# Kernel tuning notes

Hardware: AMD Instinct MI355X
Metric: run time of the kernel (lower is better)

Reference implementation:

```python
import jax, jax.numpy as jnp
import numpy as np
from jax import lax

B, CIN, COUT, H, W = 4, 256, 256, 64, 64
K, DG, STRIDE, PAD, DIL = 3, 1, 1, 1, 1
K2 = K * K
CG = CIN // DG
HO = (H + 2 * PAD - DIL * (K - 1) - 1) // STRIDE + 1
WO = (W + 2 * PAD - DIL * (K - 1) - 1) // STRIDE + 1


def setup_inputs() -> dict:
    key = jax.random.key(0)
    k1, k2, k3 = jax.random.split(key, 3)
    inputs = jax.random.normal(k1, (B, CIN, H, W), jnp.float32)
    # original init_offset() zeros these; small random weights instead so offsets ~0.5px
    w_off = jax.random.normal(k2, (3 * DG * K2, CIN, K, K), jnp.float32) * 0.01
    b_off = jnp.zeros((3 * DG * K2,), jnp.float32)
    w_dcn = jax.random.normal(k3, (COUT, CIN, K, K), jnp.float32) * (1.0 / np.sqrt(CIN * K2))
    b_dcn = jnp.zeros((COUT,), jnp.float32)
    return {"inputs": inputs, "w_off": w_off, "b_off": b_off, "w_dcn": w_dcn, "b_dcn": b_dcn}


def _conv2d(x, w, b):
    y = lax.conv_general_dilated(x, w, (STRIDE, STRIDE), [(PAD, PAD), (PAD, PAD)],
                                 rhs_dilation=(DIL, DIL),
                                 dimension_numbers=("NCHW", "OIHW", "NCHW"))
    return y + b[None, :, None, None]


def _dcn_forward(inputs, w_off, b_off, w_dcn, b_dcn):
    # offset/mask branch (standard conv), then chunk into o1, o2, mask
    om = _conv2d(inputs, w_off, b_off)                      # [B, 3*DG*K2, HO, WO]
    o1, o2, m = jnp.split(om, 3, axis=1)
    offset = jnp.concatenate([o1, o2], axis=1)              # [B, 2*DG*K2, HO, WO]
    mask = jax.nn.sigmoid(m)                                # [B, DG*K2, HO, WO]

    # DCNv2 offset layout: per deformable group, K2 taps of (dy, dx)
    off = offset.reshape(B, DG, K2, 2, HO, WO)
    dy, dx = off[:, :, :, 0], off[:, :, :, 1]               # [B, DG, K2, HO, WO]

    taps = jnp.arange(K2)
    ki = (taps // K).astype(jnp.float32)
    kj = (taps % K).astype(jnp.float32)
    hb = (jnp.arange(HO, dtype=jnp.float32) * STRIDE - PAD)
    wb = (jnp.arange(WO, dtype=jnp.float32) * STRIDE - PAD)
    py = dy + hb[None, None, None, :, None] + (ki * DIL)[None, None, :, None, None]
    px = dx + wb[None, None, None, None, :] + (kj * DIL)[None, None, :, None, None]

    y0f, x0f = jnp.floor(py), jnp.floor(px)
    ly, lx = py - y0f, px - x0f
    y0, x0 = y0f.astype(jnp.int32), x0f.astype(jnp.int32)
    y1, x1 = y0 + 1, x0 + 1

    flat = inputs.reshape(B, DG, CG, H * W)

    def corner(yi, xi, wgt):
        valid = (yi >= 0) & (yi < H) & (xi >= 0) & (xi < W)
        yc = jnp.clip(yi, 0, H - 1)
        xc = jnp.clip(xi, 0, W - 1)
        idx = (yc * W + xc).reshape(B, DG, 1, K2 * HO * WO)
        idx = jnp.broadcast_to(idx, (B, DG, CG, K2 * HO * WO))
        v = jnp.take_along_axis(flat, idx, axis=3).reshape(B, DG, CG, K2, HO, WO)
        w = jnp.where(valid, wgt, 0.0)[:, :, None]          # zero outside (zero-pad bilinear)
        return v * w

    val = (corner(y0, x0, (1 - ly) * (1 - lx)) + corner(y0, x1, (1 - ly) * lx)
           + corner(y1, x0, ly * (1 - lx)) + corner(y1, x1, ly * lx))

    cols = val * mask.reshape(B, DG, 1, K2, HO, WO)         # modulated columns
    cols = cols.reshape(B, CIN * K2, HO * WO)
    out = jnp.einsum("ok,bkn->bon", w_dcn.reshape(COUT, CIN * K2), cols)
    out = out + b_dcn[None, :, None]
    return out.reshape(B, COUT, HO, WO)


def reference(inputs, w_off, b_off, w_dcn, b_dcn):
    return _dcn_forward(inputs, w_off, b_off, w_dcn, b_dcn)
```

## Files before the change

kernel.cpp:

```cpp
#include <hip/hip_runtime.h>
#include <hip/hip_bf16.h>

typedef __bf16 bf16x8 __attribute__((ext_vector_type(8)));
typedef __bf16 bf16x4 __attribute__((ext_vector_type(4)));
typedef float f32x4 __attribute__((ext_vector_type(4)));
typedef unsigned int u32x4 __attribute__((ext_vector_type(4)));

#define CIN 256
#define COUT 256
#define KDIM 2304

__device__ __forceinline__ void gload_lds16(const void* g, void* l) {
  __builtin_amdgcn_global_load_lds(
      (__attribute__((address_space(1))) unsigned int*)g,
      (__attribute__((address_space(3))) unsigned int*)l, 16, 0, 0);
}

__global__ __launch_bounds__(256) void k_prep_all(const float* __restrict__ wdcn,
                                                  const float* __restrict__ woff,
                                                  __bf16* __restrict__ Ag,
                                                  __bf16* __restrict__ Ah,
                                                  __bf16* __restrict__ Al) {
  int bid = blockIdx.x, tid = threadIdx.x;
  if (bid < 2304) {
    int t = bid * 256 + tid;
    int cout = t / KDIM;
    int r = t - cout * KDIM;
    int tap = r >> 8, cin = r & 255;
    Ag[t] = (__bf16)wdcn[(cout * 256 + cin) * 9 + tap];
  } else {
    int t = (bid - 2304) * 256 + tid;
    int j = t & 7;
    int l = (t >> 3) & 63;
    int mh = (t >> 9) & 1;
    int s = t >> 10;
    int tap = s >> 3, cc = s & 7;
    int ki = tap / 3, kj = tap - ki * 3;
    int oc = mh * 16 + (l & 15);
    int cin = cc * 32 + ((l >> 4) << 3) + j;
    float v = (oc < 27) ? woff[((oc * 256 + cin) * 3 + ki) * 3 + kj] : 0.f;
    __bf16 hi = (__bf16)v;
    __bf16 lo = (__bf16)(v - (float)hi);
    Ah[t] = hi;
    Al[t] = lo;
  }
}

__global__ __launch_bounds__(256) void k_tr(const float* __restrict__ in,
                                            __bf16* __restrict__ inT) {
  int h = blockIdx.x, b = blockIdx.y;
  int c = threadIdx.x;
  const float* src = in + ((((b << 8) + c) << 6) + h) * 64;
  __bf16* dst = inT + (((b << 12) + (h << 6)) << 8) + c;
#pragma unroll
  for (int w4 = 0; w4 < 16; ++w4) {
    f32x4 v = *(const f32x4*)(src + (w4 << 2));
#pragma unroll
    for (int k = 0; k < 4; ++k) dst[(((w4 << 2) + k)) << 8] = (__bf16)v[k];
  }
}

__global__ __launch_bounds__(256) void k_conv(const float* __restrict__ in,
                                              const __bf16* __restrict__ Ah,
                                              const __bf16* __restrict__ Al,
                                              float* __restrict__ omp) {
  __shared__ __bf16 xh[3 * 4 * 66 * 8];
  __shared__ __bf16 xl[3 * 4 * 66 * 8];
  int tid = threadIdx.x;
  int l = tid & 63, wn = tid >> 6;
  int ho = blockIdx.x, b = blockIdx.y, ct = blockIdx.z;

  f32x4 acc[2];
  acc[0] = (f32x4){0.f, 0.f, 0.f, 0.f};
  acc[1] = (f32x4){0.f, 0.f, 0.f, 0.f};

  for (int chunk = 0; chunk < 4; ++chunk) {
    int cin0 = ct * 128 + chunk * 32;
    for (int i = tid; i < 792; i += 256) {
      int c = i % 66;
      int t2 = i / 66;
      int u = t2 & 3, r = t2 >> 2;
      int h = ho - 1 + r, w = c - 1;
      bool ok = ((unsigned)h < 64u) & ((unsigned)w < 64u);
      const float* src = in + ((((b * CIN + cin0 + u * 8) << 6) + h) << 6) + w;
      bf16x8 hv, lv;
#pragma unroll
      for (int k = 0; k < 8; ++k) {
        float v = ok ? src[k << 12] : 0.f;
        __bf16 hi = (__bf16)v;
        hv[k] = hi;
        lv[k] = (__bf16)(v - (float)hi);
      }
      int el = ((r * 4 + u) * 66 + c) << 3;
      *(bf16x8*)&xh[el] = hv;
      *(bf16x8*)&xl[el] = lv;
    }
    __syncthreads();
    int scc = ct * 4 + chunk;
#pragma unroll
    for (int tap = 0; tap < 9; ++tap) {
      int s = tap * 8 + scc;
      int ki = tap / 3, kj = tap - ki * 3;
      bf16x8 ah0 = *(const bf16x8*)(Ah + (((s * 2 + 0) * 64 + l) << 3));
      bf16x8 ah1 = *(const bf16x8*)(Ah + (((s * 2 + 1) * 64 + l) << 3));
      bf16x8 al0 = *(const bf16x8*)(Al + (((s * 2 + 0) * 64 + l) << 3));
      bf16x8 al1 = *(const bf16x8*)(Al + (((s * 2 + 1) * 64 + l) << 3));
      int u = l >> 4;
      int sc = (wn << 4) + (l & 15) + kj;
      int el = ((ki * 4 + u) * 66 + sc) << 3;
      bf16x8 bh = *(const bf16x8*)&xh[el];
      bf16x8 bl = *(const bf16x8*)&xl[el];
      acc[0] = __builtin_amdgcn_mfma_f32_16x16x32_bf16(ah0, bh, acc[0], 0, 0, 0);
      acc[1] = __builtin_amdgcn_mfma_f32_16x16x32_bf16(ah1, bh, acc[1], 0, 0, 0);
      acc[0] = __builtin_amdgcn_mfma_f32_16x16x32_bf16(al0, bh, acc[0], 0, 0, 0);
      acc[1] = __builtin_amdgcn_mfma_f32_16x16x32_bf16(al1, bh, acc[1], 0, 0, 0);
      acc[0] = __builtin_amdgcn_mfma_f32_16x16x32_bf16(ah0, bl, acc[0], 0, 0, 0);
      acc[1] = __builtin_amdgcn_mfma_f32_16x16x32_bf16(ah1, bl, acc[1], 0, 0, 0);
    }
    __syncthreads();
  }
  int n = (ho << 6) + (wn << 4) + (l & 15);
#pragma unroll
  for (int mh = 0; mh < 2; ++mh)
#pragma unroll
    for (int r = 0; r < 4; ++r) {
      int oc = mh * 16 + ((l >> 4) << 2) + r;
      if (oc < 27)
        omp[(((ct * 4 + b) * 27 + oc) << 12) + n] = acc[mh][r];
    }
}

__global__ __launch_bounds__(512, 4) void k_gemm(const __bf16* __restrict__ inT,
                                                 const float* __restrict__ omp,
                                                 const float* __restrict__ boff,
                                                 const __bf16* __restrict__ Ag,
                                                 const float* __restrict__ bdcn,
                                                 float* __restrict__ out) {
  __shared__ u32x4 sA[2048];
  __shared__ u32x4 sB[256];
  int tid = threadIdx.x;
  int l = tid & 63;
  int w = tid >> 6;
  int wm = w & 3, wh = w >> 2;
  int id = blockIdx.x;
  int x = id & 7, t = id >> 3;
  int b = x >> 1;
  int ntile = ((x & 1) << 6) + t;
  int sn = tid >> 4;
  int sc = tid & 15;
  int n_g = (ntile << 5) + sn;
  const __bf16* tb = inT + ((b << 12) << 8);

  f32x4 acc[4];
#pragma unroll
  for (int i = 0; i < 4; ++i) acc[i] = (f32x4){0.f, 0.f, 0.f, 0.f};

  float w00 = 0.f, w01 = 0.f, w10 = 0.f, w11 = 0.f;
  int o00 = 0, o01 = 0, o10 = 0, o11 = 0;

  for (int step = 0; step < 36; ++step) {
    int tap = step >> 2;
    int cin0 = (step & 3) << 6;
    if ((step & 3) == 0) {
      int ki = tap / 3, kj = tap - ki * 3;
      float dy = omp[((b * 27 + 2 * tap) << 12) + n_g] +
                 omp[(((4 + b) * 27 + 2 * tap) << 12) + n_g] + boff[2 * tap];
      float dx = omp[((b * 27 + 2 * tap + 1) << 12) + n_g] +
                 omp[(((4 + b) * 27 + 2 * tap + 1) << 12) + n_g] + boff[2 * tap + 1];
      float mv = omp[((b * 27 + 18 + tap) << 12) + n_g] +
                 omp[(((4 + b) * 27 + 18 + tap) << 12) + n_g] + boff[18 + tap];
      float msk = 1.f / (1.f + __expf(-mv));
      float py = dy + (float)((n_g >> 6) - 1 + ki);
      float px = dx + (float)((n_g & 63) - 1 + kj);
      float y0f = floorf(py), x0f = floorf(px);
      float ly = py - y0f, lx = px - x0f;
      int y0 = (int)y0f, x0 = (int)x0f;
      int y1 = y0 + 1, x1 = x0 + 1;
      bool vy0 = (y0 >= 0) & (y0 < 64), vy1 = (y1 >= 0) & (y1 < 64);
      bool vx0 = (x0 >= 0) & (x0 < 64), vx1 = (x1 >= 0) & (x1 < 64);
      float hy = 1.f - ly, hx = 1.f - lx;
      w00 = (vy0 & vx0) ? hy * hx * msk : 0.f;
      w01 = (vy0 & vx1) ? hy * lx * msk : 0.f;
      w10 = (vy1 & vx0) ? ly * hx * msk : 0.f;
      w11 = (vy1 & vx1) ? ly * lx * msk : 0.f;
      int y0c = min(max(y0, 0), 63), y1c = min(max(y1, 0), 63);
      int x0c = min(max(x0, 0), 63), x1c = min(max(x1, 0), 63);
      o00 = (y0c << 6) + x0c;
      o01 = (y0c << 6) + x1c;
      o10 = (y1c << 6) + x0c;
      o11 = (y1c << 6) + x1c;
    }
    int cbase = cin0 + (sc << 2);
    bf16x4 cA = *(const bf16x4*)(tb + (o00 << 8) + cbase);
    bf16x4 cB = *(const bf16x4*)(tb + (o01 << 8) + cbase);
    bf16x4 cC = *(const bf16x4*)(tb + (o10 << 8) + cbase);
    bf16x4 cD = *(const bf16x4*)(tb + (o11 << 8) + cbase);
    bf16x4 vv;
#pragma unroll
    for (int j = 0; j < 4; ++j) {
      float v = w00 * (float)cA[j] + w01 * (float)cB[j] + w10 * (float)cC[j] +
                w11 * (float)cD[j];
      vv[j] = (__bf16)v;
    }
    __syncthreads();
    int kk0 = (tap << 8) + cin0;
#pragma unroll
    for (int i = 0; i < 4; ++i) {
      int slot = i * 512 + tid;
      int m = slot >> 3, j = slot & 7;
      int csrc = j ^ (m & 7);
      const __bf16* src = Ag + m * KDIM + kk0 + (csrc << 3);
      gload_lds16((const void*)src, (void*)&sA[i * 512 + (tid & ~63)]);
    }
    {
      unsigned long long* sB64 = (unsigned long long*)sB;
      int slot = (sn << 3) + ((sc >> 1) ^ (sn & 7));
      sB64[slot * 2 + (sc & 1)] = __builtin_bit_cast(unsigned long long, vv);
    }
    __syncthreads();
#pragma unroll
    for (int kt = 0; kt < 2; ++kt) {
      bf16x8 af[4], bfr;
      int cc = (kt << 2) + (l >> 4);
#pragma unroll
      for (int mf = 0; mf < 4; ++mf) {
        int m = (wm << 6) + (mf << 4) + (l & 15);
        af[mf] = __builtin_bit_cast(bf16x8, sA[(m << 3) + (cc ^ (m & 7))]);
      }
      {
        int n = (wh << 4) + (l & 15);
        bfr = __builtin_bit_cast(bf16x8, sB[(n << 3) + (cc ^ (n & 7))]);
      }
#pragma unroll
      for (int mf = 0; mf < 4; ++mf)
        acc[mf] = __builtin_amdgcn_mfma_f32_16x16x32_bf16(af[mf], bfr, acc[mf],
                                                          0, 0, 0);
    }
  }
#pragma unroll
  for (int mf = 0; mf < 4; ++mf)
#pragma unroll
    for (int r = 0; r < 4; ++r) {
      int m = (wm << 6) + (mf << 4) + ((l >> 4) << 2) + r;
      int n = (ntile << 5) + (wh << 4) + (l & 15);
      out[((b * COUT + m) << 12) + n] = acc[mf][r] + bdcn[m];
    }
}

extern "C" void kernel_launch(void* const* d_in, const int* in_sizes, int n_in,
                              void* d_out, int out_size, void* d_ws, size_t ws_size,
                              hipStream_t stream) {
  const float* in = (const float*)d_in[0];
  const float* woff = (const float*)d_in[1];
  const float* boff = (const float*)d_in[2];
  const float* wdcn = (const float*)d_in[3];
  const float* bdcn = (const float*)d_in[4];
  float* out = (float*)d_out;
  char* ws = (char*)d_ws;
  __bf16* Ag = (__bf16*)ws;
  __bf16* Ah = (__bf16*)(ws + 1179648);
  __bf16* Al = (__bf16*)(ws + 1327104);
  float* omp = (float*)(ws + 1474560);
  __bf16* inT = (__bf16*)(ws + 5013504);
  k_prep_all<<<2592, 256, 0, stream>>>(wdcn, woff, Ag, Ah, Al);
  k_tr<<<dim3(64, 4), 256, 0, stream>>>(in, inT);
  k_conv<<<dim3(64, 4, 2), 256, 0, stream>>>(in, Ah, Al, omp);
  k_gemm<<<512, 512, 0, stream>>>(inT, omp, boff, Ag, bdcn, out);
}
```

Before: 93.61 us.

## Double-buffer weight tile in LDS and prefetch next-step gathers during MFMA

Doubles the shared-memory A buffer so that the next K-step's weight tile is loaded into the alternate buffer while the current step's MFMAs run. The bilinear corner gathers and offset/mask computation for the next step are also issued before the MFMA loop, so their latency overlaps with math. The second __syncthreads is replaced by an explicit lgkmcnt wait plus a raw s_barrier with scheduling barriers. In exchange, LDS per block roughly doubles, which may cut the number of resident 512-thread blocks per CU. Vector memory waits are still forced at the top-of-loop barrier, which limits how much overlap is achieved.

```diff
diff --git a/kernel.cpp b/kernel.cpp
--- a/kernel.cpp
+++ b/kernel.cpp
@@ -136,7 +136,7 @@
                                                  const __bf16* __restrict__ Ag,
                                                  const float* __restrict__ bdcn,
                                                  float* __restrict__ out) {
-  __shared__ u32x4 sA[2048];
+  __shared__ u32x4 sA[2 * 2048];
   __shared__ u32x4 sB[256];
   int tid = threadIdx.x;
   int l = tid & 63;
@@ -157,67 +157,84 @@
 
   float w00 = 0.f, w01 = 0.f, w10 = 0.f, w11 = 0.f;
   int o00 = 0, o01 = 0, o10 = 0, o11 = 0;
-
-  for (int step = 0; step < 36; ++step) {
-    int tap = step >> 2;
-    int cin0 = (step & 3) << 6;
-    if ((step & 3) == 0) {
-      int ki = tap / 3, kj = tap - ki * 3;
-      float dy = omp[((b * 27 + 2 * tap) << 12) + n_g] +
-                 omp[(((4 + b) * 27 + 2 * tap) << 12) + n_g] + boff[2 * tap];
-      float dx = omp[((b * 27 + 2 * tap + 1) << 12) + n_g] +
-                 omp[(((4 + b) * 27 + 2 * tap + 1) << 12) + n_g] + boff[2 * tap + 1];
-      float mv = omp[((b * 27 + 18 + tap) << 12) + n_g] +
-                 omp[(((4 + b) * 27 + 18 + tap) << 12) + n_g] + boff[18 + tap];
-      float msk = 1.f / (1.f + __expf(-mv));
-      float py = dy + (float)((n_g >> 6) - 1 + ki);
-      float px = dx + (float)((n_g & 63) - 1 + kj);
-      float y0f = floorf(py), x0f = floorf(px);
-      float ly = py - y0f, lx = px - x0f;
-      int y0 = (int)y0f, x0 = (int)x0f;
-      int y1 = y0 + 1, x1 = x0 + 1;
-      bool vy0 = (y0 >= 0) & (y0 < 64), vy1 = (y1 >= 0) & (y1 < 64);
-      bool vx0 = (x0 >= 0) & (x0 < 64), vx1 = (x1 >= 0) & (x1 < 64);
-      float hy = 1.f - ly, hx = 1.f - lx;
-      w00 = (vy0 & vx0) ? hy * hx * msk : 0.f;
-      w01 = (vy0 & vx1) ? hy * lx * msk : 0.f;
-      w10 = (vy1 & vx0) ? ly * hx * msk : 0.f;
-      w11 = (vy1 & vx1) ? ly * lx * msk : 0.f;
-      int y0c = min(max(y0, 0), 63), y1c = min(max(y1, 0), 63);
-      int x0c = min(max(x0, 0), 63), x1c = min(max(x1, 0), 63);
-      o00 = (y0c << 6) + x0c;
-      o01 = (y0c << 6) + x1c;
-      o10 = (y1c << 6) + x0c;
-      o11 = (y1c << 6) + x1c;
-    }
-    int cbase = cin0 + (sc << 2);
-    bf16x4 cA = *(const bf16x4*)(tb + (o00 << 8) + cbase);
-    bf16x4 cB = *(const bf16x4*)(tb + (o01 << 8) + cbase);
-    bf16x4 cC = *(const bf16x4*)(tb + (o10 << 8) + cbase);
-    bf16x4 cD = *(const bf16x4*)(tb + (o11 << 8) + cbase);
-    bf16x4 vv;
-#pragma unroll
-    for (int j = 0; j < 4; ++j) {
-      float v = w00 * (float)cA[j] + w01 * (float)cB[j] + w10 * (float)cC[j] +
-                w11 * (float)cD[j];
-      vv[j] = (__bf16)v;
-    }
-    __syncthreads();
-    int kk0 = (tap << 8) + cin0;
+  bf16x4 cA, cB, cC, cD;
+
+  auto do_corners = [&](int tap) {
+    int ki = tap / 3, kj = tap - ki * 3;
+    float dy = omp[((b * 27 + 2 * tap) << 12) + n_g] +
+               omp[(((4 + b) * 27 + 2 * tap) << 12) + n_g] + boff[2 * tap];
+    float dx = omp[((b * 27 + 2 * tap + 1) << 12) + n_g] +
+               omp[(((4 + b) * 27 + 2 * tap + 1) << 12) + n_g] + boff[2 * tap + 1];
+    float mv = omp[((b * 27 + 18 + tap) << 12) + n_g] +
+               omp[(((4 + b) * 27 + 18 + tap) << 12) + n_g] + boff[18 + tap];
+    float msk = 1.f / (1.f + __expf(-mv));
+    float py = dy + (float)((n_g >> 6) - 1 + ki);
+    float px = dx + (float)((n_g & 63) - 1 + kj);
+    float y0f = floorf(py), x0f = floorf(px);
+    float ly = py - y0f, lx = px - x0f;
+    int y0 = (int)y0f, x0 = (int)x0f;
+    int y1 = y0 + 1, x1 = x0 + 1;
+    bool vy0 = (y0 >= 0) & (y0 < 64), vy1 = (y1 >= 0) & (y1 < 64);
+    bool vx0 = (x0 >= 0) & (x0 < 64), vx1 = (x1 >= 0) & (x1 < 64);
+    float hy = 1.f - ly, hx = 1.f - lx;
+    w00 = (vy0 & vx0) ? hy * hx * msk : 0.f;
+    w01 = (vy0 & vx1) ? hy * lx * msk : 0.f;
+    w10 = (vy1 & vx0) ? ly * hx * msk : 0.f;
+    w11 = (vy1 & vx1) ? ly * lx * msk : 0.f;
+    int y0c = min(max(y0, 0), 63), y1c = min(max(y1, 0), 63);
+    int x0c = min(max(x0, 0), 63), x1c = min(max(x1, 0), 63);
+    o00 = (y0c << 6) + x0c;
+    o01 = (y0c << 6) + x1c;
+    o10 = (y1c << 6) + x0c;
+    o11 = (y1c << 6) + x1c;
+  };
+  auto do_gather = [&](int s1) {
+    int cbase = ((s1 & 3) << 6) + (sc << 2);
+    cA = *(const bf16x4*)(tb + (o00 << 8) + cbase);
+    cB = *(const bf16x4*)(tb + (o01 << 8) + cbase);
+    cC = *(const bf16x4*)(tb + (o10 << 8) + cbase);
+    cD = *(const bf16x4*)(tb + (o11 << 8) + cbase);
+  };
+  auto do_stageA = [&](int s1, int p) {
+    int kk0 = ((s1 >> 2) << 8) + ((s1 & 3) << 6);
 #pragma unroll
     for (int i = 0; i < 4; ++i) {
       int slot = i * 512 + tid;
       int m = slot >> 3, j = slot & 7;
       int csrc = j ^ (m & 7);
       const __bf16* src = Ag + m * KDIM + kk0 + (csrc << 3);
-      gload_lds16((const void*)src, (void*)&sA[i * 512 + (tid & ~63)]);
-    }
+      gload_lds16((const void*)src, (void*)&sA[p * 2048 + i * 512 + (tid & ~63)]);
+    }
+  };
+
+  do_corners(0);
+  do_stageA(0, 0);
+  do_gather(0);
+
+  for (int s = 0; s < 36; ++s) {
+    bf16x4 vv;
+#pragma unroll
+    for (int j = 0; j < 4; ++j) {
+      float v = w00 * (float)cA[j] + w01 * (float)cB[j] + w10 * (float)cC[j] +
+                w11 * (float)cD[j];
+      vv[j] = (__bf16)v;
+    }
+    __syncthreads();
+    int s1 = (s < 35) ? s + 1 : 35;
+    do_stageA(s1, (s + 1) & 1);
     {
       unsigned long long* sB64 = (unsigned long long*)sB;
       int slot = (sn << 3) + ((sc >> 1) ^ (sn & 7));
       sB64[slot * 2 + (sc & 1)] = __builtin_bit_cast(unsigned long long, vv);
     }
-    __syncthreads();
+    asm volatile("s_waitcnt lgkmcnt(0)" ::: "memory");
+    __builtin_amdgcn_sched_barrier(0);
+    __builtin_amdgcn_s_barrier();
+    __builtin_amdgcn_sched_barrier(0);
+    if (((s + 1) & 3) == 0 && s < 35) do_corners((s + 1) >> 2);
+    do_gather(s1);
+    __builtin_amdgcn_sched_barrier(0);
+    int pb = (s & 1) * 2048;
 #pragma unroll
     for (int kt = 0; kt < 2; ++kt) {
       bf16x8 af[4], bfr;
@@ -225,7 +242,7 @@
 #pragma unroll
       for (int mf = 0; mf < 4; ++mf) {
         int m = (wm << 6) + (mf << 4) + (l & 15);
-        af[mf] = __builtin_bit_cast(bf16x8, sA[(m << 3) + (cc ^ (m & 7))]);
+        af[mf] = __builtin_bit_cast(bf16x8, sA[pb + (m << 3) + (cc ^ (m & 7))]);
       }
       {
         int n = (wh << 4) + (l & 15);
```

Result: slower. 98.29 us (+5.0%).

## Feed offset conv from bf16 transposed input and drop low-part input split

Applied to the files above, without the earlier changes.

The offset/mask convolution now reads the already-transposed bf16 channel-last input (inT) with one 16-byte load per site instead of eight strided fp32 loads. It also no longer splits the input into hi/lo bf16 parts, which removes one LDS buffer and two of the six MFMAs per tap. The aim is less global and LDS traffic and fewer matrix ops in the conv kernel. In exchange the offsets lose precision because the input is now only bf16, which can move sampling positions. k_conv now also has to run after k_tr.

```diff
diff --git a/kernel.cpp b/kernel.cpp
--- a/kernel.cpp
+++ b/kernel.cpp
@@ -60,12 +60,11 @@
   }
 }
 
-__global__ __launch_bounds__(256) void k_conv(const float* __restrict__ in,
+__global__ __launch_bounds__(256) void k_conv(const __bf16* __restrict__ inT,
                                               const __bf16* __restrict__ Ah,
                                               const __bf16* __restrict__ Al,
                                               float* __restrict__ omp) {
   __shared__ __bf16 xh[3 * 4 * 66 * 8];
-  __shared__ __bf16 xl[3 * 4 * 66 * 8];
   int tid = threadIdx.x;
   int l = tid & 63, wn = tid >> 6;
   int ho = blockIdx.x, b = blockIdx.y, ct = blockIdx.z;
@@ -82,18 +81,11 @@
       int u = t2 & 3, r = t2 >> 2;
       int h = ho - 1 + r, w = c - 1;
       bool ok = ((unsigned)h < 64u) & ((unsigned)w < 64u);
-      const float* src = in + ((((b * CIN + cin0 + u * 8) << 6) + h) << 6) + w;
-      bf16x8 hv, lv;
-#pragma unroll
-      for (int k = 0; k < 8; ++k) {
-        float v = ok ? src[k << 12] : 0.f;
-        __bf16 hi = (__bf16)v;
-        hv[k] = hi;
-        lv[k] = (__bf16)(v - (float)hi);
-      }
-      int el = ((r * 4 + u) * 66 + c) << 3;
-      *(bf16x8*)&xh[el] = hv;
-      *(bf16x8*)&xl[el] = lv;
+      bf16x8 hv = (bf16x8){};
+      if (ok)
+        hv = *(const bf16x8*)(inT + ((((b << 12) + (h << 6) + w)) << 8) + cin0 +
+                              (u << 3));
+      *(bf16x8*)&xh[((r * 4 + u) * 66 + c) << 3] = hv;
     }
     __syncthreads();
     int scc = ct * 4 + chunk;
@@ -107,15 +99,11 @@
       bf16x8 al1 = *(const bf16x8*)(Al + (((s * 2 + 1) * 64 + l) << 3));
       int u = l >> 4;
       int sc = (wn << 4) + (l & 15) + kj;
-      int el = ((ki * 4 + u) * 66 + sc) << 3;
-      bf16x8 bh = *(const bf16x8*)&xh[el];
-      bf16x8 bl = *(const bf16x8*)&xl[el];
+      bf16x8 bh = *(const bf16x8*)&xh[((ki * 4 + u) * 66 + sc) << 3];
       acc[0] = __builtin_amdgcn_mfma_f32_16x16x32_bf16(ah0, bh, acc[0], 0, 0, 0);
       acc[1] = __builtin_amdgcn_mfma_f32_16x16x32_bf16(ah1, bh, acc[1], 0, 0, 0);
       acc[0] = __builtin_amdgcn_mfma_f32_16x16x32_bf16(al0, bh, acc[0], 0, 0, 0);
       acc[1] = __builtin_amdgcn_mfma_f32_16x16x32_bf16(al1, bh, acc[1], 0, 0, 0);
-      acc[0] = __builtin_amdgcn_mfma_f32_16x16x32_bf16(ah0, bl, acc[0], 0, 0, 0);
-      acc[1] = __builtin_amdgcn_mfma_f32_16x16x32_bf16(ah1, bl, acc[1], 0, 0, 0);
     }
     __syncthreads();
   }
@@ -190,17 +178,16 @@
       o10 = (y1c << 6) + x0c;
       o11 = (y1c << 6) + x1c;
     }
-    int cbase = cin0 + (sc << 2);
-    bf16x4 cA = *(const bf16x4*)(tb + (o00 << 8) + cbase);
-    bf16x4 cB = *(const bf16x4*)(tb + (o01 << 8) + cbase);
-    bf16x4 cC = *(const bf16x4*)(tb + (o10 << 8) + cbase);
-    bf16x4 cD = *(const bf16x4*)(tb + (o11 << 8) + cbase);
+    int cb0 = cin0 + (sc << 2);
+    bf16x4 cA = *(const bf16x4*)(tb + (o00 << 8) + cb0);
+    bf16x4 cB = *(const bf16x4*)(tb + (o01 << 8) + cb0);
+    bf16x4 cC = *(const bf16x4*)(tb + (o10 << 8) + cb0);
+    bf16x4 cD = *(const bf16x4*)(tb + (o11 << 8) + cb0);
     bf16x4 vv;
 #pragma unroll
     for (int j = 0; j < 4; ++j) {
-      float v = w00 * (float)cA[j] + w01 * (float)cB[j] + w10 * (float)cC[j] +
-                w11 * (float)cD[j];
-      vv[j] = (__bf16)v;
+      vv[j] = (__bf16)(w00 * (float)cA[j] + w01 * (float)cB[j] +
+                       w10 * (float)cC[j] + w11 * (float)cD[j]);
     }
     __syncthreads();
     int kk0 = (tap << 8) + cin0;
@@ -264,6 +251,6 @@
   __bf16* inT = (__bf16*)(ws + 5013504);
   k_prep_all<<<2592, 256, 0, stream>>>(wdcn, woff, Ag, Ah, Al);
   k_tr<<<dim3(64, 4), 256, 0, stream>>>(in, inT);
-  k_conv<<<dim3(64, 4, 2), 256, 0, stream>>>(in, Ah, Al, omp);
+  k_conv<<<dim3(64, 4, 2), 256, 0, stream>>>(inT, Ah, Al, omp);
   k_gemm<<<512, 512, 0, stream>>>(inT, omp, boff, Ag, bdcn, out);
 }
```

After: 93.27 us. About the same (-0.4%).
